# Optimization experiments

Hardware: AMD Instinct MI355X
Metric: run time of the kernel (lower is better)

Reference implementation:

```python
import jax, jax.numpy as jnp
import numpy as np

N = 50000      # nodes
E = 800000     # edges (avg degree 16)
VOCAB = 300    # in_dim = config['vocab_size']
EMBED = 256    # embed_dim
FC = 128       # fc_dim
NCLS = 4       # n_classes_stance
EPS = 1e-12    # F.normalize eps


def setup_inputs() -> dict:
    key = jax.random.key(0)
    ks = jax.random.split(key, 13)
    s_in = 1.0 / np.sqrt(VOCAB)
    s_h = 1.0 / np.sqrt(EMBED)
    s_fc = 1.0 / np.sqrt(FC)
    return {
        "x": jax.random.normal(ks[0], (N, VOCAB), jnp.float32),
        "edge_index": jax.random.randint(ks[1], (2, E), 0, N, dtype=jnp.int32),
        "node_mask": jnp.ones((N, 1), dtype=bool),
        # SAGEConv 1: lin_l (neighbor, with bias) and lin_r (root, no bias)
        "w1_l": jax.random.normal(ks[2], (EMBED, VOCAB), jnp.float32) * s_in,
        "b1_l": jnp.zeros((EMBED,), jnp.float32),
        "w1_r": jax.random.normal(ks[3], (EMBED, VOCAB), jnp.float32) * s_in,
        # SAGEConv 2
        "w2_l": jax.random.normal(ks[4], (EMBED, EMBED), jnp.float32) * s_h,
        "b2_l": jnp.zeros((EMBED,), jnp.float32),
        "w2_r": jax.random.normal(ks[5], (EMBED, EMBED), jnp.float32) * s_h,
        # classifier_stance MLP
        "cw1": jax.random.normal(ks[6], (FC, EMBED), jnp.float32) * s_h,
        "cb1": jnp.zeros((FC,), jnp.float32),
        "cw2": jax.random.normal(ks[7], (NCLS, FC), jnp.float32) * s_fc,
        "cb2": jnp.zeros((NCLS,), jnp.float32),
    }


def _sage_conv(x, src, dst, w_l, b_l, w_r):
    # mean aggregation of source-node features onto destinations
    msg = x[src]                                              # [E, d] gather
    s = jax.ops.segment_sum(msg, dst, num_segments=N)         # [N, d] scatter-add
    cnt = jax.ops.segment_sum(jnp.ones((src.shape[0], 1), x.dtype), dst,
                              num_segments=N)                 # [N, 1]
    agg = s / jnp.maximum(cnt, 1.0)
    h = agg @ w_l.T + b_l + x @ w_r.T                         # lin_l(agg)+lin_r(x)
    # normalize=True -> L2 normalize rows (F.normalize semantics)
    n = jnp.linalg.norm(h, axis=-1, keepdims=True)
    return h / jnp.maximum(n, EPS)


def reference(x, edge_index, node_mask, w1_l, b1_l, w1_r, w2_l, b2_l, w2_r,
              cw1, cb1, cw2, cb2):
    # eval mode: node_drop mask not applied, dropout is identity
    src, dst = edge_index[0], edge_index[1]
    h = jax.nn.relu(_sage_conv(x, src, dst, w1_l, b1_l, w1_r))
    h2 = _sage_conv(h, src, dst, w2_l, b2_l, w2_r)
    out = jax.nn.relu(h2 @ cw1.T + cb1) @ cw2.T + cb2         # classifier_stance
    return (out, node_mask, h2)
```

## Files before the change

kernel.cpp:

```cpp
#include <hip/hip_runtime.h>

constexpr int NN = 50000;
constexpr int MP = 50048;
constexpr int NE = 800000;
constexpr int KV = 300;
constexpr int KP1 = 320;
constexpr int DE = 256;
constexpr int DF = 128;
constexpr int NC = 4;

typedef __attribute__((ext_vector_type(8))) short bf16x8;
typedef __attribute__((ext_vector_type(4))) float f32x4;

__device__ inline float b2f(ushort u) { return __uint_as_float((uint)u << 16); }
__device__ inline ushort f2b(float f) {
    uint u = __float_as_uint(f);
    u += 0x7fffu + ((u >> 16) & 1u);
    return (ushort)(u >> 16);
}
__device__ inline void gload_lds16(const void* g, void* l) {
    __builtin_amdgcn_global_load_lds(
        (const __attribute__((address_space(1))) void*)g,
        (__attribute__((address_space(3))) void*)l, 16, 0, 0);
}

__global__ __launch_bounds__(256) void k_degree(const int* __restrict__ dst,
                                                int* __restrict__ deg) {
    int e = blockIdx.x * 256 + threadIdx.x;
    if (e < NE) atomicAdd(&deg[dst[e]], 1);
}

__global__ __launch_bounds__(256) void k_scan1(const int* __restrict__ deg,
                                               int* __restrict__ partial) {
    __shared__ int sd[256];
    int t = threadIdx.x;
    int n = blockIdx.x * 256 + t;
    sd[t] = (n < NN) ? deg[n] : 0;
    __syncthreads();
    for (int off = 128; off > 0; off >>= 1) {
        if (t < off) sd[t] += sd[t + off];
        __syncthreads();
    }
    if (t == 0) partial[blockIdx.x] = sd[0];
}

__global__ __launch_bounds__(256) void k_scan2(const int* __restrict__ partial,
                                               int* __restrict__ poff, int nb) {
    __shared__ int sd[256];
    int t = threadIdx.x;
    int v = (t < nb) ? partial[t] : 0;
    sd[t] = v;
    __syncthreads();
    for (int off = 1; off < 256; off <<= 1) {
        int x = (t >= off) ? sd[t - off] : 0;
        __syncthreads();
        sd[t] += x;
        __syncthreads();
    }
    poff[t] = sd[t] - v;
}

__global__ __launch_bounds__(256) void k_scan3(const int* __restrict__ deg,
                                               const int* __restrict__ poff,
                                               int* __restrict__ rowptr) {
    __shared__ int sd[256];
    int t = threadIdx.x;
    int n = blockIdx.x * 256 + t;
    int v = (n < NN) ? deg[n] : 0;
    sd[t] = v;
    __syncthreads();
    for (int off = 1; off < 256; off <<= 1) {
        int x = (t >= off) ? sd[t - off] : 0;
        __syncthreads();
        sd[t] += x;
        __syncthreads();
    }
    if (n < NN) rowptr[n] = poff[blockIdx.x] + sd[t] - v;
    if (blockIdx.x == 0 && t == 0) rowptr[NN] = NE;
}

__global__ __launch_bounds__(256) void k_scatter(const int* __restrict__ src,
                                                 const int* __restrict__ dst,
                                                 const int* __restrict__ rowptr,
                                                 int* __restrict__ cnt2,
                                                 int* __restrict__ col) {
    int e = blockIdx.x * 256 + threadIdx.x;
    if (e < NE) {
        int d = dst[e];
        int p = rowptr[d] + atomicAdd(&cnt2[d], 1);
        col[p] = src[e];
    }
}

__global__ __launch_bounds__(256) void k_cvt_x(const float* __restrict__ x,
                                               ushort* __restrict__ xb) {
    int i = blockIdx.x * 256 + threadIdx.x;
    if (i >= MP * (KP1 / 8)) return;
    int row = i / (KP1 / 8);
    int kb = (i % (KP1 / 8)) * 8;
    float f[8] = {0.f, 0.f, 0.f, 0.f, 0.f, 0.f, 0.f, 0.f};
    if (row < NN) {
        const float* s = x + (size_t)row * KV + kb;
        if (kb + 8 <= KV) {
            float4 v0 = *(const float4*)s;
            float4 v1 = *(const float4*)(s + 4);
            f[0] = v0.x; f[1] = v0.y; f[2] = v0.z; f[3] = v0.w;
            f[4] = v1.x; f[5] = v1.y; f[6] = v1.z; f[7] = v1.w;
        } else {
#pragma unroll
            for (int j = 0; j < 8; ++j)
                if (kb + j < KV) f[j] = s[j];
        }
    }
    ushort v[8];
#pragma unroll
    for (int j = 0; j < 8; ++j) v[j] = f2b(f[j]);
    uint4 pk;
    pk.x = (uint)v[0] | ((uint)v[1] << 16);
    pk.y = (uint)v[2] | ((uint)v[3] << 16);
    pk.z = (uint)v[4] | ((uint)v[5] << 16);
    pk.w = (uint)v[6] | ((uint)v[7] << 16);
    *(uint4*)(xb + (size_t)row * KP1 + kb) = pk;
}

__global__ __launch_bounds__(256) void k_cvt_w(const float* __restrict__ w,
                                               ushort* __restrict__ o,
                                               int rows, int Kin, int KPr) {
    int i = blockIdx.x * 256 + threadIdx.x;
    if (i >= rows * (KPr / 8)) return;
    int row = i / (KPr / 8);
    int kb = (i % (KPr / 8)) * 8;
    const float* s = w + (size_t)row * Kin + kb;
    float f[8] = {0.f, 0.f, 0.f, 0.f, 0.f, 0.f, 0.f, 0.f};
    if (kb + 8 <= Kin) {
        float4 v0 = *(const float4*)s;
        float4 v1 = *(const float4*)(s + 4);
        f[0] = v0.x; f[1] = v0.y; f[2] = v0.z; f[3] = v0.w;
        f[4] = v1.x; f[5] = v1.y; f[6] = v1.z; f[7] = v1.w;
    } else {
#pragma unroll
        for (int j = 0; j < 8; ++j)
            if (kb + j < Kin) f[j] = s[j];
    }
    ushort v[8];
#pragma unroll
    for (int j = 0; j < 8; ++j) v[j] = f2b(f[j]);
    uint4 pk;
    pk.x = (uint)v[0] | ((uint)v[1] << 16);
    pk.y = (uint)v[2] | ((uint)v[3] << 16);
    pk.z = (uint)v[4] | ((uint)v[5] << 16);
    pk.w = (uint)v[6] | ((uint)v[7] << 16);
    *(uint4*)(o + (size_t)row * KPr + kb) = pk;
}

__global__ __launch_bounds__(256) void k_mgemm(const ushort* __restrict__ A,
                                               const ushort* __restrict__ B,
                                               ushort* __restrict__ C,
                                               int KPr, int Nst,
                                               const float* __restrict__ bias,
                                               int relu) {
    __shared__ __align__(16) ushort As[128 * 64];
    __shared__ __align__(16) ushort Bs[128 * 64];
    const int t = threadIdx.x;
    const int bn = blockIdx.x * 128;
    const int bm = blockIdx.y * 128;
    const int w = t >> 6;
    const int lane = t & 63;
    const int wr = (w >> 1) * 64, wc = (w & 1) * 64;
    const int fr = lane & 15;
    const int fg = lane >> 4;
    const int drow = (lane >> 4) * 4;
    const int dcol = lane & 15;

    f32x4 acc[4][4];
#pragma unroll
    for (int m = 0; m < 4; ++m)
#pragma unroll
        for (int n = 0; n < 4; ++n) acc[m][n] = (f32x4){0.f, 0.f, 0.f, 0.f};

    const int srow = lane >> 3;
    const int sblk = (lane & 7) ^ srow;
    const ushort* Ab = A + (size_t)(bm + w * 32 + srow) * KPr + sblk * 8;
    const ushort* Bb = B + (size_t)(bn + w * 32 + srow) * KPr + sblk * 8;
    ushort* Al = As + w * 2048 + lane * 8;
    ushort* Bl = Bs + w * 2048 + lane * 8;

    for (int k0 = 0; k0 < KPr; k0 += 64) {
#pragma unroll
        for (int j = 0; j < 4; ++j) {
            gload_lds16(Ab + k0 + (size_t)j * 8 * KPr, Al + j * 512);
            gload_lds16(Bb + k0 + (size_t)j * 8 * KPr, Bl + j * 512);
        }
        __syncthreads();
#pragma unroll
        for (int ks = 0; ks < 2; ++ks) {
            bf16x8 af[4], bfr[4];
#pragma unroll
            for (int m = 0; m < 4; ++m) {
                int row = wr + 16 * m + fr;
                int blk = (fg + 4 * ks) ^ (row & 7);
                af[m] = *(const bf16x8*)(As + row * 64 + blk * 8);
            }
#pragma unroll
            for (int n = 0; n < 4; ++n) {
                int row = wc + 16 * n + fr;
                int blk = (fg + 4 * ks) ^ (row & 7);
                bfr[n] = *(const bf16x8*)(Bs + row * 64 + blk * 8);
            }
#pragma unroll
            for (int m = 0; m < 4; ++m)
#pragma unroll
                for (int n = 0; n < 4; ++n)
                    acc[m][n] = __builtin_amdgcn_mfma_f32_16x16x32_bf16(
                        af[m], bfr[n], acc[m][n], 0, 0, 0);
        }
        __syncthreads();
    }
#pragma unroll
    for (int m = 0; m < 4; ++m) {
        int gr0 = bm + wr + 16 * m + drow;
#pragma unroll
        for (int n = 0; n < 4; ++n) {
            int gc = bn + wc + 16 * n + dcol;
            float bv = bias ? bias[gc] : 0.f;
#pragma unroll
            for (int r = 0; r < 4; ++r) {
                float v = acc[m][n][r] + bv;
                if (relu) v = fmaxf(v, 0.f);
                C[(size_t)(gr0 + r) * Nst + gc] = f2b(v);
            }
        }
    }
}

__global__ __launch_bounds__(256) void k_aggnorm(const ushort* __restrict__ Cmat,
                                                 const float* __restrict__ bias,
                                                 const int* __restrict__ rowptr,
                                                 const int* __restrict__ col,
                                                 float* __restrict__ outf,
                                                 ushort* __restrict__ outb,
                                                 int relu) {
    int wave = threadIdx.x >> 6;
    int lane = threadIdx.x & 63;
    int n = blockIdx.x * 4 + wave;
    if (n >= NN) return;
    int beg = rowptr[n], end = rowptr[n + 1];
    const ushort* base = Cmat + (size_t)lane * 4;
    float a0 = 0.f, a1 = 0.f, a2 = 0.f, a3 = 0.f;
    float c0 = 0.f, c1 = 0.f, c2 = 0.f, c3 = 0.f;
    int e = beg;
    for (; e + 4 <= end; e += 4) {
        int s0 = col[e], s1 = col[e + 1], s2 = col[e + 2], s3 = col[e + 3];
        ushort4 v0 = *(const ushort4*)(base + (size_t)s0 * 512);
        ushort4 v1 = *(const ushort4*)(base + (size_t)s1 * 512);
        ushort4 v2 = *(const ushort4*)(base + (size_t)s2 * 512);
        ushort4 v3 = *(const ushort4*)(base + (size_t)s3 * 512);
        a0 += b2f(v0.x); a1 += b2f(v0.y); a2 += b2f(v0.z); a3 += b2f(v0.w);
        c0 += b2f(v1.x); c1 += b2f(v1.y); c2 += b2f(v1.z); c3 += b2f(v1.w);
        a0 += b2f(v2.x); a1 += b2f(v2.y); a2 += b2f(v2.z); a3 += b2f(v2.w);
        c0 += b2f(v3.x); c1 += b2f(v3.y); c2 += b2f(v3.z); c3 += b2f(v3.w);
    }
    for (; e < end; ++e) {
        int s = col[e];
        ushort4 v = *(const ushort4*)(base + (size_t)s * 512);
        a0 += b2f(v.x); a1 += b2f(v.y); a2 += b2f(v.z); a3 += b2f(v.w);
    }
    a0 += c0; a1 += c1; a2 += c2; a3 += c3;
    int d = end - beg;
    float inv = 1.0f / (float)(d > 1 ? d : 1);
    ushort4 rv = *(const ushort4*)(Cmat + (size_t)n * 512 + 256 + lane * 4);
    float4 b = *(const float4*)(bias + lane * 4);
    float hx = a0 * inv + b.x + b2f(rv.x);
    float hy = a1 * inv + b.y + b2f(rv.y);
    float hz = a2 * inv + b.z + b2f(rv.z);
    float hw = a3 * inv + b.w + b2f(rv.w);
    float ss = hx * hx + hy * hy + hz * hz + hw * hw;
#pragma unroll
    for (int off = 32; off > 0; off >>= 1) ss += __shfl_xor(ss, off, 64);
    float scale = 1.0f / fmaxf(sqrtf(ss), 1e-12f);
    hx *= scale; hy *= scale; hz *= scale; hw *= scale;
    if (relu) {
        hx = fmaxf(hx, 0.f); hy = fmaxf(hy, 0.f);
        hz = fmaxf(hz, 0.f); hw = fmaxf(hw, 0.f);
    }
    if (outf) {
        float4 o = make_float4(hx, hy, hz, hw);
        *(float4*)(outf + (size_t)n * DE + lane * 4) = o;
    }
    ushort4 ob;
    ob.x = f2b(hx); ob.y = f2b(hy); ob.z = f2b(hz); ob.w = f2b(hw);
    *(ushort4*)(outb + (size_t)n * DE + lane * 4) = ob;
}

__global__ __launch_bounds__(256) void k_out(const ushort* __restrict__ hid,
                                             const float* __restrict__ cw2,
                                             const float* __restrict__ cb2,
                                             float* __restrict__ outp) {
    int wave = threadIdx.x >> 6;
    int lane = threadIdx.x & 63;
    int n = blockIdx.x * 4 + wave;
    if (n >= NN) return;
    uint hv = *(const uint*)(hid + (size_t)n * DF + lane * 2);
    float h0 = b2f((ushort)(hv & 0xffff));
    float h1 = b2f((ushort)(hv >> 16));
    float p0 = h0 * cw2[0 * DF + 2 * lane] + h1 * cw2[0 * DF + 2 * lane + 1];
    float p1 = h0 * cw2[1 * DF + 2 * lane] + h1 * cw2[1 * DF + 2 * lane + 1];
    float p2 = h0 * cw2[2 * DF + 2 * lane] + h1 * cw2[2 * DF + 2 * lane + 1];
    float p3 = h0 * cw2[3 * DF + 2 * lane] + h1 * cw2[3 * DF + 2 * lane + 1];
#pragma unroll
    for (int off = 32; off > 0; off >>= 1) {
        p0 += __shfl_xor(p0, off, 64);
        p1 += __shfl_xor(p1, off, 64);
        p2 += __shfl_xor(p2, off, 64);
        p3 += __shfl_xor(p3, off, 64);
    }
    if (lane == 0) {
        outp[(size_t)n * NC + 0] = p0 + cb2[0];
        outp[(size_t)n * NC + 1] = p1 + cb2[1];
        outp[(size_t)n * NC + 2] = p2 + cb2[2];
        outp[(size_t)n * NC + 3] = p3 + cb2[3];
    }
}

__global__ __launch_bounds__(256) void k_mask(const unsigned char* __restrict__ m8,
                                              float* __restrict__ o) {
    int i = blockIdx.x * 256 + threadIdx.x;
    if (i >= NN) return;
    bool bytes = (m8[1] != 0);
    float v;
    if (bytes) v = (m8[i] != 0) ? 1.0f : 0.0f;
    else       v = (((const int*)m8)[i] != 0) ? 1.0f : 0.0f;
    o[i] = v;
}

extern "C" void kernel_launch(void* const* d_in, const int* in_sizes, int n_in,
                              void* d_out, int out_size, void* d_ws, size_t ws_size,
                              hipStream_t stream) {
    const float* x   = (const float*)d_in[0];
    const int*   ei  = (const int*)d_in[1];
    const void*  msk = d_in[2];
    const float* w1l = (const float*)d_in[3];
    const float* b1l = (const float*)d_in[4];
    const float* w1r = (const float*)d_in[5];
    const float* w2l = (const float*)d_in[6];
    const float* b2l = (const float*)d_in[7];
    const float* w2r = (const float*)d_in[8];
    const float* cw1 = (const float*)d_in[9];
    const float* cb1 = (const float*)d_in[10];
    const float* cw2 = (const float*)d_in[11];
    const float* cb2 = (const float*)d_in[12];

    float* out        = (float*)d_out;
    float* out_logits = out;
    float* out_mask   = out + (size_t)NN * NC;
    float* h2f        = out + (size_t)NN * NC + NN;

    char* wp = (char*)d_ws;
    auto alloc = [&](size_t bytes) -> void* {
        void* p = (void*)wp;
        wp += (bytes + 255) & ~(size_t)255;
        return p;
    };
    int* counters = (int*)alloc((size_t)2 * NN * 4);
    int* deg  = counters;
    int* cnt2 = counters + NN;
    int* rowptr  = (int*)alloc((size_t)(NN + 1) * 4);
    int* partial = (int*)alloc(256 * 4);
    int* poff    = (int*)alloc(256 * 4);
    int* col     = (int*)alloc((size_t)NE * 4);
    ushort* xb    = (ushort*)alloc((size_t)MP * KP1 * 2);
    ushort* wcat1 = (ushort*)alloc((size_t)512 * KP1 * 2);
    ushort* wcat2 = (ushort*)alloc((size_t)512 * DE * 2);
    ushort* cw1b  = (ushort*)alloc((size_t)DF * DE * 2);
    ushort* Cbuf  = (ushort*)alloc((size_t)MP * 512 * 2);
    ushort* h1b   = (ushort*)alloc((size_t)MP * DE * 2);
    ushort* h2b   = (ushort*)alloc((size_t)MP * DE * 2);
    ushort* hidb  = (ushort*)alloc((size_t)MP * DF * 2);

    const int* srcp = ei;
    const int* dstp = ei + NE;

    hipMemsetAsync(counters, 0, (size_t)2 * NN * 4, stream);
    k_degree<<<(NE + 255) / 256, 256, 0, stream>>>(dstp, deg);
    int nb = (NN + 255) / 256;
    k_scan1<<<nb, 256, 0, stream>>>(deg, partial);
    k_scan2<<<1, 256, 0, stream>>>(partial, poff, nb);
    k_scan3<<<nb, 256, 0, stream>>>(deg, poff, rowptr);
    k_scatter<<<(NE + 255) / 256, 256, 0, stream>>>(srcp, dstp, rowptr, cnt2, col);

    k_cvt_x<<<(MP * (KP1 / 8) + 255) / 256, 256, 0, stream>>>(x, xb);
    k_cvt_w<<<(256 * (KP1 / 8) + 255) / 256, 256, 0, stream>>>(w1l, wcat1, 256, KV, KP1);
    k_cvt_w<<<(256 * (KP1 / 8) + 255) / 256, 256, 0, stream>>>(w1r, wcat1 + (size_t)256 * KP1, 256, KV, KP1);
    k_cvt_w<<<(256 * (DE / 8) + 255) / 256, 256, 0, stream>>>(w2l, wcat2, 256, DE, DE);
    k_cvt_w<<<(256 * (DE / 8) + 255) / 256, 256, 0, stream>>>(w2r, wcat2 + (size_t)256 * DE, 256, DE, DE);
    k_cvt_w<<<(DF * (DE / 8) + 255) / 256, 256, 0, stream>>>(cw1, cw1b, DF, DE, DE);

    dim3 g1(512 / 128, MP / 128);
    k_mgemm<<<g1, 256, 0, stream>>>(xb, wcat1, Cbuf, KP1, 512, nullptr, 0);
    k_aggnorm<<<NN / 4, 256, 0, stream>>>(Cbuf, b1l, rowptr, col, nullptr, h1b, 1);
    k_mgemm<<<g1, 256, 0, stream>>>(h1b, wcat2, Cbuf, DE, 512, nullptr, 0);
    k_aggnorm<<<NN / 4, 256, 0, stream>>>(Cbuf, b2l, rowptr, col, h2f, h2b, 0);

    dim3 g2(DF / 128, MP / 128);
    k_mgemm<<<g2, 256, 0, stream>>>(h2b, cw1b, hidb, DE, DF, cb1, 1);
    k_out<<<(NN + 3) / 4, 256, 0, stream>>>(hidb, cw2, cb2, out_logits);
    k_mask<<<(NN + 255) / 256, 256, 0, stream>>>((const unsigned char*)msk, out_mask);
}
```

Measured before the change: 468.0 us.

## Store neighbor projections in FP8 for gather, fuse classifier MLP, merge weight casts

The layer GEMM now writes the neighbor-projection half as FP8 bytes into a separate buffer and the root half as bf16, so the edge gather in the aggregation kernel reads 256 bytes per neighbor instead of 512. The aggregation loop is unrolled to 8 edges. The classifier's second GEMM and the 4-class output projection are fused into one kernel that keeps the hidden tile in LDS, and the five weight-conversion launches are merged into one. FP8 quantization of the messages adds precision loss and may risk the accuracy tolerance.

```diff
diff --git a/kernel.cpp b/kernel.cpp
--- a/kernel.cpp
+++ b/kernel.cpp
@@ -123,14 +123,24 @@
     *(uint4*)(xb + (size_t)row * KP1 + kb) = pk;
 }
 
-__global__ __launch_bounds__(256) void k_cvt_w(const float* __restrict__ w,
-                                               ushort* __restrict__ o,
-                                               int rows, int Kin, int KPr) {
+__global__ __launch_bounds__(256) void k_cvt_wall(const float* __restrict__ w1l,
+                                                  const float* __restrict__ w1r,
+                                                  const float* __restrict__ w2l,
+                                                  const float* __restrict__ w2r,
+                                                  const float* __restrict__ cw1,
+                                                  ushort* __restrict__ wcat1,
+                                                  ushort* __restrict__ wcat2,
+                                                  ushort* __restrict__ cw1b) {
     int i = blockIdx.x * 256 + threadIdx.x;
-    if (i >= rows * (KPr / 8)) return;
-    int row = i / (KPr / 8);
-    int kb = (i % (KPr / 8)) * 8;
-    const float* s = w + (size_t)row * Kin + kb;
+    const float* src; ushort* dst; int row, kb, Kin;
+    if (i < 10240)            { int g = i;          row = g / 40; kb = (g % 40) * 8; src = w1l; dst = wcat1;                       Kin = KV; }
+    else if (i < 20480)       { int g = i - 10240;  row = g / 40; kb = (g % 40) * 8; src = w1r; dst = wcat1 + (size_t)256 * KP1;   Kin = KV; }
+    else if (i < 28672)       { int g = i - 20480;  row = g / 32; kb = (g % 32) * 8; src = w2l; dst = wcat2;                       Kin = DE; }
+    else if (i < 36864)       { int g = i - 28672;  row = g / 32; kb = (g % 32) * 8; src = w2r; dst = wcat2 + (size_t)256 * DE;    Kin = DE; }
+    else if (i < 40960)       { int g = i - 36864;  row = g / 32; kb = (g % 32) * 8; src = cw1; dst = cw1b;                        Kin = DE; }
+    else return;
+    int KPr = (Kin == KV) ? KP1 : DE;
+    const float* s = src + (size_t)row * Kin + kb;
     float f[8] = {0.f, 0.f, 0.f, 0.f, 0.f, 0.f, 0.f, 0.f};
     if (kb + 8 <= Kin) {
         float4 v0 = *(const float4*)s;
@@ -150,15 +160,14 @@
     pk.y = (uint)v[2] | ((uint)v[3] << 16);
     pk.z = (uint)v[4] | ((uint)v[5] << 16);
     pk.w = (uint)v[6] | ((uint)v[7] << 16);
-    *(uint4*)(o + (size_t)row * KPr + kb) = pk;
-}
-
-__global__ __launch_bounds__(256) void k_mgemm(const ushort* __restrict__ A,
-                                               const ushort* __restrict__ B,
-                                               ushort* __restrict__ C,
-                                               int KPr, int Nst,
-                                               const float* __restrict__ bias,
-                                               int relu) {
+    *(uint4*)(dst + (size_t)row * KPr + kb) = pk;
+}
+
+__global__ __launch_bounds__(256) void k_mgemm_layer(const ushort* __restrict__ A,
+                                                     const ushort* __restrict__ B,
+                                                     unsigned char* __restrict__ ybuf,
+                                                     ushort* __restrict__ yrb,
+                                                     int KPr) {
     __shared__ __align__(16) ushort As[128 * 64];
     __shared__ __align__(16) ushort Bs[128 * 64];
     const int t = threadIdx.x;
@@ -222,18 +231,128 @@
 #pragma unroll
         for (int n = 0; n < 4; ++n) {
             int gc = bn + wc + 16 * n + dcol;
-            float bv = bias ? bias[gc] : 0.f;
 #pragma unroll
             for (int r = 0; r < 4; ++r) {
-                float v = acc[m][n][r] + bv;
-                if (relu) v = fmaxf(v, 0.f);
-                C[(size_t)(gr0 + r) * Nst + gc] = f2b(v);
+                float v = acc[m][n][r];
+                if (gc < 256) {
+                    uint p = __builtin_amdgcn_cvt_pk_fp8_f32(v, v, 0, false);
+                    ybuf[(size_t)(gr0 + r) * 256 + gc] = (unsigned char)(p & 0xff);
+                } else {
+                    yrb[(size_t)(gr0 + r) * 256 + (gc - 256)] = f2b(v);
+                }
             }
         }
     }
 }
 
-__global__ __launch_bounds__(256) void k_aggnorm(const ushort* __restrict__ Cmat,
+__global__ __launch_bounds__(256) void k_mcls(const ushort* __restrict__ A,
+                                              const ushort* __restrict__ B,
+                                              const float* __restrict__ cb1,
+                                              const float* __restrict__ cw2,
+                                              const float* __restrict__ cb2,
+                                              float* __restrict__ outp) {
+    __shared__ __align__(16) ushort smem[128 * 130];
+    __shared__ float cw2s[NC * DF];
+    ushort* As = smem;
+    ushort* Bs = smem + 8192;
+    const int t = threadIdx.x;
+    const int bm = blockIdx.y * 128;
+    const int w = t >> 6;
+    const int lane = t & 63;
+    const int wr = (w >> 1) * 64, wc = (w & 1) * 64;
+    const int fr = lane & 15;
+    const int fg = lane >> 4;
+    const int drow = (lane >> 4) * 4;
+    const int dcol = lane & 15;
+
+    for (int i = t; i < NC * DF; i += 256) cw2s[i] = cw2[i];
+
+    f32x4 acc[4][4];
+#pragma unroll
+    for (int m = 0; m < 4; ++m)
+#pragma unroll
+        for (int n = 0; n < 4; ++n) acc[m][n] = (f32x4){0.f, 0.f, 0.f, 0.f};
+
+    const int srow = lane >> 3;
+    const int sblk = (lane & 7) ^ srow;
+    const ushort* Ab = A + (size_t)(bm + w * 32 + srow) * DE + sblk * 8;
+    const ushort* Bb = B + (size_t)(w * 32 + srow) * DE + sblk * 8;
+    ushort* Al = As + w * 2048 + lane * 8;
+    ushort* Bl = Bs + w * 2048 + lane * 8;
+
+    for (int k0 = 0; k0 < DE; k0 += 64) {
+#pragma unroll
+        for (int j = 0; j < 4; ++j) {
+            gload_lds16(Ab + k0 + (size_t)j * 8 * DE, Al + j * 512);
+            gload_lds16(Bb + k0 + (size_t)j * 8 * DE, Bl + j * 512);
+        }
+        __syncthreads();
+#pragma unroll
+        for (int ks = 0; ks < 2; ++ks) {
+            bf16x8 af[4], bfr[4];
+#pragma unroll
+            for (int m = 0; m < 4; ++m) {
+                int row = wr + 16 * m + fr;
+                int blk = (fg + 4 * ks) ^ (row & 7);
+                af[m] = *(const bf16x8*)(As + row * 64 + blk * 8);
+            }
+#pragma unroll
+            for (int n = 0; n < 4; ++n) {
+                int row = wc + 16 * n + fr;
+                int blk = (fg + 4 * ks) ^ (row & 7);
+                bfr[n] = *(const bf16x8*)(Bs + row * 64 + blk * 8);
+            }
+#pragma unroll
+            for (int m = 0; m < 4; ++m)
+#pragma unroll
+                for (int n = 0; n < 4; ++n)
+                    acc[m][n] = __builtin_amdgcn_mfma_f32_16x16x32_bf16(
+                        af[m], bfr[n], acc[m][n], 0, 0, 0);
+        }
+        __syncthreads();
+    }
+#pragma unroll
+    for (int m = 0; m < 4; ++m) {
+        int lr0 = wr + 16 * m + drow;
+#pragma unroll
+        for (int n = 0; n < 4; ++n) {
+            int f = wc + 16 * n + dcol;
+            float bv = cb1[f];
+#pragma unroll
+            for (int r = 0; r < 4; ++r) {
+                float v = fmaxf(acc[m][n][r] + bv, 0.f);
+                smem[(lr0 + r) * 130 + f] = f2b(v);
+            }
+        }
+    }
+    __syncthreads();
+    int node = t >> 1;
+    int half = t & 1;
+    float p0 = 0.f, p1 = 0.f, p2 = 0.f, p3 = 0.f;
+#pragma unroll
+    for (int i = 0; i < 32; ++i) {
+        uint hv = *(const uint*)&smem[node * 130 + half * 64 + 2 * i];
+        float h0 = b2f((ushort)(hv & 0xffff));
+        float h1 = b2f((ushort)(hv >> 16));
+        int f = half * 64 + 2 * i;
+        p0 += h0 * cw2s[0 * DF + f] + h1 * cw2s[0 * DF + f + 1];
+        p1 += h0 * cw2s[1 * DF + f] + h1 * cw2s[1 * DF + f + 1];
+        p2 += h0 * cw2s[2 * DF + f] + h1 * cw2s[2 * DF + f + 1];
+        p3 += h0 * cw2s[3 * DF + f] + h1 * cw2s[3 * DF + f + 1];
+    }
+    p0 += __shfl_xor(p0, 1, 64);
+    p1 += __shfl_xor(p1, 1, 64);
+    p2 += __shfl_xor(p2, 1, 64);
+    p3 += __shfl_xor(p3, 1, 64);
+    int ng = bm + node;
+    if (half == 0 && ng < NN) {
+        float4 o = make_float4(p0 + cb2[0], p1 + cb2[1], p2 + cb2[2], p3 + cb2[3]);
+        *(float4*)(outp + (size_t)ng * NC) = o;
+    }
+}
+
+__global__ __launch_bounds__(256) void k_aggnorm(const uint* __restrict__ yl,
+                                                 const ushort* __restrict__ yrb,
                                                  const float* __restrict__ bias,
                                                  const int* __restrict__ rowptr,
                                                  const int* __restrict__ col,
@@ -245,30 +364,37 @@
     int n = blockIdx.x * 4 + wave;
     if (n >= NN) return;
     int beg = rowptr[n], end = rowptr[n + 1];
-    const ushort* base = Cmat + (size_t)lane * 4;
+    const uint* base = yl + lane;
     float a0 = 0.f, a1 = 0.f, a2 = 0.f, a3 = 0.f;
     float c0 = 0.f, c1 = 0.f, c2 = 0.f, c3 = 0.f;
     int e = beg;
-    for (; e + 4 <= end; e += 4) {
-        int s0 = col[e], s1 = col[e + 1], s2 = col[e + 2], s3 = col[e + 3];
-        ushort4 v0 = *(const ushort4*)(base + (size_t)s0 * 512);
-        ushort4 v1 = *(const ushort4*)(base + (size_t)s1 * 512);
-        ushort4 v2 = *(const ushort4*)(base + (size_t)s2 * 512);
-        ushort4 v3 = *(const ushort4*)(base + (size_t)s3 * 512);
-        a0 += b2f(v0.x); a1 += b2f(v0.y); a2 += b2f(v0.z); a3 += b2f(v0.w);
-        c0 += b2f(v1.x); c1 += b2f(v1.y); c2 += b2f(v1.z); c3 += b2f(v1.w);
-        a0 += b2f(v2.x); a1 += b2f(v2.y); a2 += b2f(v2.z); a3 += b2f(v2.w);
-        c0 += b2f(v3.x); c1 += b2f(v3.y); c2 += b2f(v3.z); c3 += b2f(v3.w);
+    for (; e + 8 <= end; e += 8) {
+        uint v[8];
+#pragma unroll
+        for (int j = 0; j < 8; ++j) v[j] = base[(size_t)col[e + j] * 64];
+#pragma unroll
+        for (int j = 0; j < 8; j += 2) {
+            a0 += __builtin_amdgcn_cvt_f32_fp8(v[j], 0);
+            a1 += __builtin_amdgcn_cvt_f32_fp8(v[j], 1);
+            a2 += __builtin_amdgcn_cvt_f32_fp8(v[j], 2);
+            a3 += __builtin_amdgcn_cvt_f32_fp8(v[j], 3);
+            c0 += __builtin_amdgcn_cvt_f32_fp8(v[j + 1], 0);
+            c1 += __builtin_amdgcn_cvt_f32_fp8(v[j + 1], 1);
+            c2 += __builtin_amdgcn_cvt_f32_fp8(v[j + 1], 2);
+            c3 += __builtin_amdgcn_cvt_f32_fp8(v[j + 1], 3);
+        }
     }
     for (; e < end; ++e) {
-        int s = col[e];
-        ushort4 v = *(const ushort4*)(base + (size_t)s * 512);
-        a0 += b2f(v.x); a1 += b2f(v.y); a2 += b2f(v.z); a3 += b2f(v.w);
+        uint v = base[(size_t)col[e] * 64];
+        a0 += __builtin_amdgcn_cvt_f32_fp8(v, 0);
+        a1 += __builtin_amdgcn_cvt_f32_fp8(v, 1);
+        a2 += __builtin_amdgcn_cvt_f32_fp8(v, 2);
+        a3 += __builtin_amdgcn_cvt_f32_fp8(v, 3);
     }
     a0 += c0; a1 += c1; a2 += c2; a3 += c3;
     int d = end - beg;
     float inv = 1.0f / (float)(d > 1 ? d : 1);
-    ushort4 rv = *(const ushort4*)(Cmat + (size_t)n * 512 + 256 + lane * 4);
+    ushort4 rv = *(const ushort4*)(yrb + (size_t)n * 256 + lane * 4);
     float4 b = *(const float4*)(bias + lane * 4);
     float hx = a0 * inv + b.x + b2f(rv.x);
     float hy = a1 * inv + b.y + b2f(rv.y);
@@ -290,36 +416,6 @@
     ushort4 ob;
     ob.x = f2b(hx); ob.y = f2b(hy); ob.z = f2b(hz); ob.w = f2b(hw);
     *(ushort4*)(outb + (size_t)n * DE + lane * 4) = ob;
-}
-
-__global__ __launch_bounds__(256) void k_out(const ushort* __restrict__ hid,
-                                             const float* __restrict__ cw2,
-                                             const float* __restrict__ cb2,
-                                             float* __restrict__ outp) {
-    int wave = threadIdx.x >> 6;
-    int lane = threadIdx.x & 63;
-    int n = blockIdx.x * 4 + wave;
-    if (n >= NN) return;
-    uint hv = *(const uint*)(hid + (size_t)n * DF + lane * 2);
-    float h0 = b2f((ushort)(hv & 0xffff));
-    float h1 = b2f((ushort)(hv >> 16));
-    float p0 = h0 * cw2[0 * DF + 2 * lane] + h1 * cw2[0 * DF + 2 * lane + 1];
-    float p1 = h0 * cw2[1 * DF + 2 * lane] + h1 * cw2[1 * DF + 2 * lane + 1];
-    float p2 = h0 * cw2[2 * DF + 2 * lane] + h1 * cw2[2 * DF + 2 * lane + 1];
-    float p3 = h0 * cw2[3 * DF + 2 * lane] + h1 * cw2[3 * DF + 2 * lane + 1];
-#pragma unroll
-    for (int off = 32; off > 0; off >>= 1) {
-        p0 += __shfl_xor(p0, off, 64);
-        p1 += __shfl_xor(p1, off, 64);
-        p2 += __shfl_xor(p2, off, 64);
-        p3 += __shfl_xor(p3, off, 64);
-    }
-    if (lane == 0) {
-        outp[(size_t)n * NC + 0] = p0 + cb2[0];
-        outp[(size_t)n * NC + 1] = p1 + cb2[1];
-        outp[(size_t)n * NC + 2] = p2 + cb2[2];
-        outp[(size_t)n * NC + 3] = p3 + cb2[3];
-    }
 }
 
 __global__ __launch_bounds__(256) void k_mask(const unsigned char* __restrict__ m8,
@@ -372,10 +468,10 @@
     ushort* wcat1 = (ushort*)alloc((size_t)512 * KP1 * 2);
     ushort* wcat2 = (ushort*)alloc((size_t)512 * DE * 2);
     ushort* cw1b  = (ushort*)alloc((size_t)DF * DE * 2);
-    ushort* Cbuf  = (ushort*)alloc((size_t)MP * 512 * 2);
+    unsigned char* ybuf = (unsigned char*)alloc((size_t)MP * 256);
+    ushort* yrb   = (ushort*)alloc((size_t)MP * 256 * 2);
     ushort* h1b   = (ushort*)alloc((size_t)MP * DE * 2);
     ushort* h2b   = (ushort*)alloc((size_t)MP * DE * 2);
-    ushort* hidb  = (ushort*)alloc((size_t)MP * DF * 2);
 
     const int* srcp = ei;
     const int* dstp = ei + NE;
@@ -389,20 +485,18 @@
     k_scatter<<<(NE + 255) / 256, 256, 0, stream>>>(srcp, dstp, rowptr, cnt2, col);
 
     k_cvt_x<<<(MP * (KP1 / 8) + 255) / 256, 256, 0, stream>>>(x, xb);
-    k_cvt_w<<<(256 * (KP1 / 8) + 255) / 256, 256, 0, stream>>>(w1l, wcat1, 256, KV, KP1);
-    k_cvt_w<<<(256 * (KP1 / 8) + 255) / 256, 256, 0, stream>>>(w1r, wcat1 + (size_t)256 * KP1, 256, KV, KP1);
-    k_cvt_w<<<(256 * (DE / 8) + 255) / 256, 256, 0, stream>>>(w2l, wcat2, 256, DE, DE);
-    k_cvt_w<<<(256 * (DE / 8) + 255) / 256, 256, 0, stream>>>(w2r, wcat2 + (size_t)256 * DE, 256, DE, DE);
-    k_cvt_w<<<(DF * (DE / 8) + 255) / 256, 256, 0, stream>>>(cw1, cw1b, DF, DE, DE);
+    k_cvt_wall<<<(40960 + 255) / 256, 256, 0, stream>>>(w1l, w1r, w2l, w2r, cw1,
+                                                        wcat1, wcat2, cw1b);
 
     dim3 g1(512 / 128, MP / 128);
-    k_mgemm<<<g1, 256, 0, stream>>>(xb, wcat1, Cbuf, KP1, 512, nullptr, 0);
-    k_aggnorm<<<NN / 4, 256, 0, stream>>>(Cbuf, b1l, rowptr, col, nullptr, h1b, 1);
-    k_mgemm<<<g1, 256, 0, stream>>>(h1b, wcat2, Cbuf, DE, 512, nullptr, 0);
-    k_aggnorm<<<NN / 4, 256, 0, stream>>>(Cbuf, b2l, rowptr, col, h2f, h2b, 0);
-
-    dim3 g2(DF / 128, MP / 128);
-    k_mgemm<<<g2, 256, 0, stream>>>(h2b, cw1b, hidb, DE, DF, cb1, 1);
-    k_out<<<(NN + 3) / 4, 256, 0, stream>>>(hidb, cw2, cb2, out_logits);
+    k_mgemm_layer<<<g1, 256, 0, stream>>>(xb, wcat1, ybuf, yrb, KP1);
+    k_aggnorm<<<NN / 4, 256, 0, stream>>>((const uint*)ybuf, yrb, b1l, rowptr, col,
+                                          nullptr, h1b, 1);
+    k_mgemm_layer<<<g1, 256, 0, stream>>>(h1b, wcat2, ybuf, yrb, DE);
+    k_aggnorm<<<NN / 4, 256, 0, stream>>>((const uint*)ybuf, yrb, b2l, rowptr, col,
+                                          h2f, h2b, 0);
+
+    dim3 g2(1, MP / 128);
+    k_mcls<<<g2, 256, 0, stream>>>(h2b, cw1b, cb1, cw2, cb2, out_logits);
     k_mask<<<(NN + 255) / 256, 256, 0, stream>>>((const unsigned char*)msk, out_mask);
 }
```

After: 401.5 us. 1.17x faster.
